# Performance work log

Hardware: AMD Instinct MI355X
Metric: run time of the kernel (lower is better)

## Reference

```python
import jax, jax.numpy as jnp
import numpy as np

N_QUBITS = 10
N_LAYERS = 3
DIM = 2 ** N_QUBITS
B = 2048
T1, T2, GATE_TIME = 0.05, 0.07, 1e-07
P_GATE_1Q, P_GATE_2Q, P_READOUT = 0.001, 0.01, 0.02
P_AMP = 1.0 - np.exp(-GATE_TIME / T1)
P_PHASE = 1.0 - np.exp(-GATE_TIME / T2)

_I = np.eye(2, dtype=np.complex64)
_X = np.array([[0, 1], [1, 0]], np.complex64)
_Y = np.array([[0, -1j], [1j, 0]], np.complex64)
_Z = np.array([[1, 0], [0, -1]], np.complex64)

def _depol(p):
    return [np.sqrt(1 - p) * _I, np.sqrt(p / 3) * _X, np.sqrt(p / 3) * _Y, np.sqrt(p / 3) * _Z]

def _ampdamp(g):
    return [np.array([[1, 0], [0, np.sqrt(1 - g)]], np.complex64), np.array([[0, np.sqrt(g)], [0, 0]], np.complex64)]

def _phasedamp(g):
    return [np.array([[1, 0], [0, np.sqrt(1 - g)]], np.complex64), np.array([[0, 0], [0, np.sqrt(g)]], np.complex64)]

def _bitflip(p):
    return [np.sqrt(1 - p) * _I, np.sqrt(p) * _X]

DEPOL1 = [jnp.asarray(k) for k in _depol(P_GATE_1Q)]
DEPOL2 = [jnp.asarray(k) for k in _depol(P_GATE_2Q)]
AMP = [jnp.asarray(k) for k in _ampdamp(P_AMP)]
PHASE = [jnp.asarray(k) for k in _phasedamp(P_PHASE)]
BITFLIP = [jnp.asarray(k) for k in _bitflip(P_READOUT)]
CNOT = jnp.asarray(np.array([[1, 0, 0, 0], [0, 1, 0, 0], [0, 0, 0, 1], [0, 0, 1, 0]], np.complex64).reshape(2, 2, 2, 2))

def pauli_strings(n):
    out = []
    for q in range(n):
        for ch in 'XZ':
            out.append('I' * q + ch + 'I' * (n - q - 1))
    return out

def pauli_tensor(strings):
    mats = {'I': np.eye(2), 'X': np.array([[0., 1.], [1., 0.]]), 'Z': np.array([[1., 0.], [0., -1.]])}
    Ps = []
    for s in strings:
        P = np.array([[1.0]])
        for ch in s:
            P = np.kron(P, mats[ch])
        Ps.append(P)
    return np.stack(Ps).astype(np.float32)

def _apply1(rho, K, q, n):
    # rho' = K rho K^dagger on wire q; rho has shape (2,)*2n (ket axes 0..n-1, bra axes n..2n-1)
    rho = jnp.moveaxis(jnp.tensordot(K, rho, axes=[[1], [q]]), 0, q)
    rho = jnp.moveaxis(jnp.tensordot(jnp.conj(K), rho, axes=[[1], [n + q]]), 0, n + q)
    return rho

def _apply2(rho, U, q1, q2, n):
    rho = jnp.moveaxis(jnp.tensordot(U, rho, axes=[[2, 3], [q1, q2]]), [0, 1], [q1, q2])
    rho = jnp.moveaxis(jnp.tensordot(jnp.conj(U), rho, axes=[[2, 3], [n + q1, n + q2]]), [0, 1], [n + q1, n + q2])
    return rho

def _chan1(rho, Ks, q, n):
    out = _apply1(rho, Ks[0], q, n)
    for K in Ks[1:]:
        out = out + _apply1(rho, K, q, n)
    return out

def _rot(phi, theta, omega):
    # qml.Rot = RZ(omega) @ RY(theta) @ RZ(phi)
    c = jnp.cos(theta / 2).astype(jnp.complex64)
    s = jnp.sin(theta / 2).astype(jnp.complex64)
    ep = jnp.exp(-0.5j * (phi + omega))
    em = jnp.exp(0.5j * (phi - omega))
    return jnp.stack([jnp.stack([ep * c, -em * s]), jnp.stack([jnp.conj(em) * s, jnp.conj(ep) * c])])

def _simulate(weights):
    nl, nq, _ = weights.shape
    rho = jnp.zeros((2,) * (2 * nq), jnp.complex64).at[(0,) * (2 * nq)].set(1.0)
    for l in range(nl):
        for q in range(nq):
            rho = _apply1(rho, _rot(weights[l, q, 0], weights[l, q, 1], weights[l, q, 2]), q, nq)
            rho = _chan1(rho, DEPOL1, q, nq)
            rho = _chan1(rho, AMP, q, nq)
            rho = _chan1(rho, PHASE, q, nq)
        for q in range(nq):
            t = (q + 1) % nq
            rho = _apply2(rho, CNOT, q, t, nq)
            for wq in (q, t):
                rho = _chan1(rho, DEPOL2, wq, nq)
            for wq in (q, t):
                rho = _chan1(rho, AMP, wq, nq)
            for wq in (q, t):
                rho = _chan1(rho, PHASE, wq, nq)
    for q in range(nq):
        rho = _chan1(rho, BITFLIP, q, nq)
    return rho.reshape(2 ** nq, 2 ** nq)

def setup_inputs() -> dict:
    key = jax.random.key(0)
    k1, k2, k3 = jax.random.split(key, 3)
    x = jax.random.normal(k1, (B, DIM), jnp.float32)
    circuit_weights = jax.random.uniform(k2, (N_LAYERS, N_QUBITS, 3), jnp.float32)
    w = jax.random.normal(k3, (2 * N_QUBITS,), jnp.float32) * 0.01
    b = jnp.zeros((DIM,), jnp.float32)
    P_tensor = jnp.asarray(pauli_tensor(pauli_strings(N_QUBITS)))  # [K, dim, dim]
    return {"x": x, "b": b, "w": w, "circuit_weights": circuit_weights, "P_tensor": P_tensor}

def reference(x, b, w, circuit_weights, P_tensor):
    x_t = x + b  # [B, dim]
    feats = jnp.einsum('bm,kmn,bn->bk', x_t, P_tensor, x_t)  # [B, K]
    rho = _simulate(circuit_weights)  # [dim, dim] complex
    exps = jnp.real(jnp.einsum('kmn,nm->k', P_tensor.astype(jnp.complex64), rho))  # tr(P_k rho)
    logits = jnp.sum(feats * (w * exps), axis=1)
    return jax.nn.sigmoid(logits)
```

## Files before the change

kernel.cpp:

```cpp
#include <hip/hip_runtime.h>
#include <hip/hip_bf16.h>
#include <math.h>

struct cf { float x, y; };
__device__ __forceinline__ cf cfmul(cf a, cf b){ return {a.x*b.x - a.y*b.y, a.x*b.y + a.y*b.x}; }
__device__ __forceinline__ cf cfconj(cf a){ return {a.x, -a.y}; }
__device__ __forceinline__ cf cfadd(cf a, cf b){ return {a.x+b.x, a.y+b.y}; }

__device__ __forceinline__ void pmat(int k, cf* P){
    if (k==0){ P[0]={1.f,0.f}; P[1]={0.f,0.f}; P[2]={0.f,0.f}; P[3]={1.f,0.f}; }
    else if (k==1){ P[0]={0.f,0.f}; P[1]={1.f,0.f}; P[2]={1.f,0.f}; P[3]={0.f,0.f}; }
    else if (k==2){ P[0]={0.f,0.f}; P[1]={0.f,-1.f}; P[2]={0.f,1.f}; P[3]={0.f,0.f}; }
    else { P[0]={1.f,0.f}; P[1]={0.f,0.f}; P[2]={0.f,0.f}; P[3]={-1.f,0.f}; }
}
__device__ void mul2(cf* C, const cf* A, const cf* B){
    C[0]=cfadd(cfmul(A[0],B[0]),cfmul(A[1],B[2]));
    C[1]=cfadd(cfmul(A[0],B[1]),cfmul(A[1],B[3]));
    C[2]=cfadd(cfmul(A[2],B[0]),cfmul(A[3],B[2]));
    C[3]=cfadd(cfmul(A[2],B[1]),cfmul(A[3],B[3]));
}
__device__ void ptm_acc(float* T, const cf* K){
    cf Kd[4] = {cfconj(K[0]), cfconj(K[2]), cfconj(K[1]), cfconj(K[3])};
    for (int s=0;s<4;s++){
        cf Ps[4]; pmat(s,Ps);
        cf t1[4], t2[4];
        mul2(t1, K, Ps);
        mul2(t2, t1, Kd);
        for (int t=0;t<4;t++){
            cf Pt[4]; pmat(t,Pt);
            float re = Pt[0].x*t2[0].x - Pt[0].y*t2[0].y
                     + Pt[1].x*t2[2].x - Pt[1].y*t2[2].y
                     + Pt[2].x*t2[1].x - Pt[2].y*t2[1].y
                     + Pt[3].x*t2[3].x - Pt[3].y*t2[3].y;
            T[t*4+s] += 0.5f*re;
        }
    }
}
__device__ void rmm4(float* C, const float* A, const float* B){
    for (int i=0;i<4;i++) for (int j=0;j<4;j++){
        float s=0.f;
        for (int k=0;k<4;k++) s += A[i*4+k]*B[k*4+j];
        C[i*4+j]=s;
    }
}

__device__ void prep_compute(float* sm, const float* __restrict__ wts, int tid){
    if (tid < 31){
        const float GA = -expm1f(-2.0000000000000002e-06f);
        const float GP = -expm1f(-1.4285714285714286e-06f);
        float sa = sqrtf(1.f-GA), spp = sqrtf(1.f-GP);
        float p = (tid==30) ? 0.01f : 0.001f;
        float f = 1.f - (4.f/3.f)*p;
        float Tn[16] = {0};
        Tn[0]      = 1.f;
        Tn[1*4+1]  = spp*sa*f;
        Tn[2*4+2]  = spp*sa*f;
        Tn[3*4+3]  = (1.f-GA)*f;
        Tn[3*4+0]  = GA;
        if (tid == 30){
            for (int i=0;i<16;i++) sm[480+i] = Tn[i];
        } else {
            float phi = wts[tid*3+0], th = wts[tid*3+1], om = wts[tid*3+2];
            float ct = cosf(0.5f*th), st = sinf(0.5f*th);
            cf ep = {cosf(0.5f*(phi+om)), -sinf(0.5f*(phi+om))};
            cf em = {cosf(0.5f*(phi-om)),  sinf(0.5f*(phi-om))};
            cf U[4];
            U[0] = { ep.x*ct,  ep.y*ct};
            U[1] = {-em.x*st, -em.y*st};
            U[2] = { em.x*st, -em.y*st};
            U[3] = { ep.x*ct, -ep.y*ct};
            float Tr[16] = {0};
            ptm_acc(Tr, U);
            float S[16]; rmm4(S, Tn, Tr);
            for (int i=0;i<16;i++) sm[tid*16+i] = S[i];
        }
    }
}

__device__ __forceinline__ unsigned swz(unsigned t){ return t ^ ((t>>7)&0x1Cu); }

#define ALONG_A(Mp) { _Pragma("unroll") for (int db_=0; db_<4; db_++){ \
    float a0=v[db_], a1=v[4+db_], a2=v[8+db_], a3=v[12+db_]; \
    _Pragma("unroll") for (int dp_=0; dp_<4; dp_++){ \
        v[dp_*4+db_] = (Mp)[dp_*4+0]*a0 + (Mp)[dp_*4+1]*a1 + (Mp)[dp_*4+2]*a2 + (Mp)[dp_*4+3]*a3; } } }

#define ALONG_B(Mp) { _Pragma("unroll") for (int da_=0; da_<4; da_++){ \
    float a0=v[da_*4+0], a1=v[da_*4+1], a2=v[da_*4+2], a3=v[da_*4+3]; \
    _Pragma("unroll") for (int dp_=0; dp_<4; dp_++){ \
        v[da_*4+dp_] = (Mp)[dp_*4+0]*a0 + (Mp)[dp_*4+1]*a1 + (Mp)[dp_*4+2]*a2 + (Mp)[dp_*4+3]*a3; } } }

#define ALONG_AT(Mp) { _Pragma("unroll") for (int db_=0; db_<4; db_++){ \
    float a0=v[db_], a1=v[4+db_], a2=v[8+db_], a3=v[12+db_]; \
    _Pragma("unroll") for (int dp_=0; dp_<4; dp_++){ \
        v[dp_*4+db_] = (Mp)[0*4+dp_]*a0 + (Mp)[1*4+dp_]*a1 + (Mp)[2*4+dp_]*a2 + (Mp)[3*4+dp_]*a3; } } }

#define ALONG_BT(Mp) { _Pragma("unroll") for (int da_=0; da_<4; da_++){ \
    float a0=v[da_*4+0], a1=v[da_*4+1], a2=v[da_*4+2], a3=v[da_*4+3]; \
    _Pragma("unroll") for (int dp_=0; dp_<4; dp_++){ \
        v[da_*4+dp_] = (Mp)[0*4+dp_]*a0 + (Mp)[1*4+dp_]*a1 + (Mp)[2*4+dp_]*a2 + (Mp)[3*4+dp_]*a3; } } }

#define CNOT_PERM { float t0; \
    t0=v[4];  v[4]=v[5];   v[5]=t0;  \
    t0=v[8];  v[8]=v[9];   v[9]=t0;  \
    t0=v[2];  v[2]=v[14];  v[14]=t0; \
    t0=v[3];  v[3]=v[15];  v[15]=t0; \
    t0=v[6];  v[6]=v[11];  v[11]=t0; \
    t0=v[7];  v[7]=-v[10]; v[10]=-t0; }

__device__ __constant__ const int cA_PA[5] = {0,10,8,6,4}, cA_PB[5] = {10,8,6,4,2};
__device__ __constant__ const int cB_PA[5] = {2,10,8,6,4}, cB_PB[5] = {10,8,6,4,0};

template<int LAYER, int ISB>
__device__ __forceinline__ void run_ops(float* tile, const float* sm, int tid){
#pragma unroll
    for (int i=0; i<5; i++){
        const int pa = ISB ? cB_PA[i] : cA_PA[i];
        const int pb = ISB ? cB_PB[i] : cA_PB[i];
        const int mA = (!ISB && i==0) ? LAYER*160 : -1;
        const int mB = !ISB ? (LAYER*10 + i + 1)*16
                            : ((i < 4) ? (LAYER*10 + 6 + i)*16 : -1);
        const int lo = pa < pb ? pa : pb, hi = pa < pb ? pb : pa;
        unsigned g8 = (unsigned)tid;
        unsigned xx = ((g8 >> lo) << (lo+2)) | (g8 & ((1u<<lo)-1u));
        xx = ((xx >> hi) << (hi+2)) | (xx & ((1u<<hi)-1u));
        unsigned adr[16];
        float v[16];
#pragma unroll
        for (int d=0; d<16; d++){
            unsigned t = xx | ((unsigned)(d>>2) << pa) | ((unsigned)(d&3) << pb);
            adr[d] = swz(t);
            v[d] = tile[adr[d]];
        }
        if (mA >= 0){ const float* M = sm + mA; ALONG_A(M); }
        if (mB >= 0){ const float* M = sm + mB; ALONG_B(M); }
        CNOT_PERM
        { const float* M = sm + 480; ALONG_B(M); ALONG_A(M); }
#pragma unroll
        for (int d=0; d<16; d++) tile[adr[d]] = v[d];
        __syncthreads();
    }
}

__global__ void __launch_bounds__(512, 1)
phase0_dual(float* __restrict__ rho, const float* __restrict__ wts,
            float* __restrict__ smg, float* __restrict__ Vbuf)
{
    __shared__ __align__(16) float tileS[4096];
    __shared__ __align__(16) float tileV[4096];
    __shared__ __align__(16) float sm[496];
    int tid = threadIdx.x;
    unsigned blk = blockIdx.x;
    const bool lower = (tid < 256);
    const int lt = tid & 255;

    prep_compute(sm, wts, tid);

    if (lower){
        unsigned bo = blk << 12;
#pragma unroll
        for (int r=0; r<16; r++){
            unsigned u = lt + 256u*r;
            unsigned g = u | bo;
            unsigned e = g & 0x55555u, o = (g>>1) & 0x55555u;
            tileS[swz(u)] = (e==o) ? 1.f : 0.f;
        }
    } else if (blk < 12){
        int k = (int)blk;
        unsigned sk = ((k & 1) ? 3u : 1u) << (2*(k>>1));
#pragma unroll
        for (int r=0; r<16; r++){
            unsigned u = lt + 256u*r;
            tileV[swz(u)] = (u == sk) ? 1.f : 0.f;
        }
    }
    __syncthreads();

    if (blk == 0 && lower && lt < 124)
        reinterpret_cast<float4*>(smg)[lt] = *reinterpret_cast<const float4*>(&sm[4*lt]);

#pragma unroll
    for (int it=0; it<5; ++it){
        if (lower){
            const int i = it;
            const int pa = cA_PA[i], pb = cA_PB[i];
            const int mA = (i==0) ? 0 : -1;
            const int mB = (i + 1)*16;
            const int lo = pa < pb ? pa : pb, hi = pa < pb ? pb : pa;
            unsigned g8 = (unsigned)lt;
            unsigned xx = ((g8 >> lo) << (lo+2)) | (g8 & ((1u<<lo)-1u));
            xx = ((xx >> hi) << (hi+2)) | (xx & ((1u<<hi)-1u));
            unsigned adr[16];
            float v[16];
#pragma unroll
            for (int d=0; d<16; d++){
                unsigned t = xx | ((unsigned)(d>>2) << pa) | ((unsigned)(d&3) << pb);
                adr[d] = swz(t);
                v[d] = tileS[adr[d]];
            }
            if (mA >= 0){ const float* M = sm + mA; ALONG_A(M); }
            { const float* M = sm + mB; ALONG_B(M); }
            CNOT_PERM
            { const float* M = sm + 480; ALONG_B(M); ALONG_A(M); }
#pragma unroll
            for (int d=0; d<16; d++) tileS[adr[d]] = v[d];
        } else if (blk < 12){
            const int i = 4 - it;
            const int pa = cB_PA[i], pb = cB_PB[i];
            const int mB = (i < 4) ? (26 + i)*16 : -1;
            const int lo = pa < pb ? pa : pb, hi = pa < pb ? pb : pa;
            unsigned g8 = (unsigned)lt;
            unsigned xx = ((g8 >> lo) << (lo+2)) | (g8 & ((1u<<lo)-1u));
            xx = ((xx >> hi) << (hi+2)) | (xx & ((1u<<hi)-1u));
            unsigned adr[16];
            float v[16];
#pragma unroll
            for (int d=0; d<16; d++){
                unsigned t = xx | ((unsigned)(d>>2) << pa) | ((unsigned)(d&3) << pb);
                adr[d] = swz(t);
                v[d] = tileV[adr[d]];
            }
            { const float* M = sm + 480; ALONG_AT(M); ALONG_BT(M); }
            CNOT_PERM
            if (mB >= 0){ const float* M = sm + mB; ALONG_BT(M); }
#pragma unroll
            for (int d=0; d<16; d++) tileV[adr[d]] = v[d];
        }
        __syncthreads();
    }

    if (lower){
        unsigned bo = blk << 12;
#pragma unroll
        for (int r=0; r<4; r++){
            unsigned u = 4u*(lt + 256u*r);
            *reinterpret_cast<float4*>(rho + (u | bo)) =
                *reinterpret_cast<const float4*>(&tileS[swz(u)]);
        }
    } else if (blk < 12){
#pragma unroll
        for (int r=0; r<4; r++){
            unsigned u = 4u*(lt + 256u*r);
            *reinterpret_cast<float4*>(Vbuf + (int)blk*4096 + u) =
                *reinterpret_cast<const float4*>(&tileV[swz(u)]);
        }
    }
}

template<int LAYER, int ISB, int MODE>
__global__ void __launch_bounds__(256)
fused6(float* __restrict__ rho, const float* __restrict__ smg, float* __restrict__ cvec,
       const float* __restrict__ Vbuf, float* __restrict__ part)
{
    __shared__ __align__(16) float tile[4096];
    __shared__ __align__(16) float sm[496];
    __shared__ float redp[192];
    int tid = threadIdx.x;
    unsigned blk = blockIdx.x;

    if (tid < 124)
        reinterpret_cast<float4*>(sm)[tid] = reinterpret_cast<const float4*>(smg)[tid];

    unsigned bo = blk << (ISB ? 4 : 12);
#pragma unroll
    for (int r=0; r<4; r++){
        unsigned u = 4u*(tid + 256u*r);
        unsigned g = ISB ? ((u & 15u) | ((u>>4)<<12) | bo) : (u | bo);
        *reinterpret_cast<float4*>(&tile[swz(u)]) = *reinterpret_cast<const float4*>(rho + g);
    }
    __syncthreads();

    run_ops<LAYER, ISB>(tile, sm, tid);

    if (MODE == 3){
        if (blk == 0 && tid < 8){
            const unsigned TI[8] = {1024u,3072u,256u,768u,64u,192u,16u,48u};
            cvec[2 + tid] = tile[swz(TI[tid])];
        }
        if (tid < 192){
            int k = tid >> 4, j = tid & 15;
            redp[tid] = Vbuf[k*4096 + (int)blk*16 + j] * tile[j];
        }
        __syncthreads();
        if (tid < 12){
            float s = 0.f;
#pragma unroll
            for (int j=0; j<16; j++) s += redp[tid*16 + j];
            part[tid*256 + (int)blk] = s;
        }
        return;
    }

#pragma unroll
    for (int r=0; r<4; r++){
        unsigned u = 4u*(tid + 256u*r);
        unsigned g = ISB ? ((u & 15u) | ((u>>4)<<12) | bo) : (u | bo);
        *reinterpret_cast<float4*>(rho + g) = *reinterpret_cast<const float4*>(&tile[swz(u)]);
    }
}

__global__ void __launch_bounds__(256)
logits_mega(const float* __restrict__ part, const float* __restrict__ cvec,
            const float* __restrict__ x, const float* __restrict__ bvec,
            const float* __restrict__ w, float* __restrict__ out)
{
    __shared__ float xs[1024];
    __shared__ float cvw[20];
    __shared__ float redl[80];
    __shared__ float redp[192];
    int tid = threadIdx.x;
    int b = (int)blockIdx.x;

    if (tid < 192){
        int k = tid >> 4, j = tid & 15;
        float s = 0.f;
#pragma unroll
        for (int m=0; m<16; m++) s += part[k*256 + j*16 + m];
        redp[tid] = s;
    }
    {
        float4 xv = reinterpret_cast<const float4*>(x + (size_t)b*1024)[tid];
        float4 bv = reinterpret_cast<const float4*>(bvec)[tid];
        xs[tid*4+0] = xv.x + bv.x;
        xs[tid*4+1] = xv.y + bv.y;
        xs[tid*4+2] = xv.z + bv.z;
        xs[tid*4+3] = xv.w + bv.w;
    }
    __syncthreads();
    if (tid < 12){
        float s = 0.f;
#pragma unroll
        for (int j=0; j<16; j++) s += redp[tid*16 + j];
        const int TQ[6] = {0,5,9,8,7,6};
        int ci = 2*TQ[tid>>1] + (tid & 1);
        cvw[ci] = ((tid & 1) ? 0.96f : 1.0f) * w[ci] * s;
    } else if (tid < 20){
        int ci = tid - 10;
        cvw[ci] = ((ci & 1) ? 0.96f : 1.0f) * w[ci] * cvec[ci];
    }

    float aX[10] = {0,0,0,0,0,0,0,0,0,0};
    float aZ[10] = {0,0,0,0,0,0,0,0,0,0};
#pragma unroll
    for (int r=0; r<4; r++){
        int m = tid + r*256;
        float xm = xs[m];
        float x2 = xm*xm;
#pragma unroll
        for (int q=0; q<10; q++){
            int bit = 1 << (9-q);
            aX[q] += xm * xs[m ^ bit];
            aZ[q] += (m & bit) ? -x2 : x2;
        }
    }
    int lane = tid & 63, wv = tid >> 6;
#pragma unroll
    for (int kk=0; kk<20; kk++){
        float v = (kk < 10) ? aX[kk] : aZ[kk-10];
        v += __shfl_down(v, 32); v += __shfl_down(v, 16); v += __shfl_down(v, 8);
        v += __shfl_down(v, 4);  v += __shfl_down(v, 2);  v += __shfl_down(v, 1);
        if (lane == 0) redl[wv*20 + kk] = v;
    }
    __syncthreads();
    if (tid == 0){
        float logit = 0.f;
#pragma unroll
        for (int q=0; q<10; q++){
            float FX = redl[q]    + redl[20+q] + redl[40+q] + redl[60+q];
            float FZ = redl[10+q] + redl[30+q] + redl[50+q] + redl[70+q];
            logit += cvw[2*q] * FX + cvw[2*q+1] * FZ;
        }
        out[b] = 1.f / (1.f + expf(-logit));
    }
}

extern "C" void kernel_launch(void* const* d_in, const int* in_sizes, int n_in,
                              void* d_out, int out_size, void* d_ws, size_t ws_size,
                              hipStream_t stream) {
    const float* x    = (const float*)d_in[0];
    const float* bvec = (const float*)d_in[1];
    const float* w    = (const float*)d_in[2];
    const float* cw   = (const float*)d_in[3];
    float* out = (float*)d_out;

    char* ws = (char*)d_ws;
    float* rho  = (float*)ws;
    float* smg  = (float*)(ws + (size_t)(1u<<20)*sizeof(float));
    float* cvec = smg + 512;
    float* part = cvec + 32;
    float* Vbuf = part + 3072;
    (void)ws_size; (void)in_sizes; (void)n_in; (void)out_size;

    phase0_dual<<<256, 512, 0, stream>>>(rho, cw, smg, Vbuf);
    fused6<0,1,0><<<256, 256, 0, stream>>>(rho, smg, cvec, Vbuf, part);
    fused6<1,0,0><<<256, 256, 0, stream>>>(rho, smg, cvec, Vbuf, part);
    fused6<1,1,0><<<256, 256, 0, stream>>>(rho, smg, cvec, Vbuf, part);
    fused6<2,0,3><<<256, 256, 0, stream>>>(rho, smg, cvec, Vbuf, part);
    logits_mega<<<2048, 256, 0, stream>>>(part, cvec, x, bvec, w, out);
}
```

Measured before the change: 67.96 us.

## Fold last circuit layer into precomputed adjoint observables to drop one pass

Removes the final fused6 launch, which applied the last layer to the full density matrix. Instead, phase0 precomputes extra back-propagated basis tensors (P4Tbuf, VAbuf), and the third-layer kernel contracts its tile against them to produce all twenty expectation partials directly. This saves one full read-modify-write pass over rho and one launch. In exchange it adds a heavier per-block contraction (a 16x16 inner product per output plus 12 Vbuf reads per element) and more precompute blocks in phase0.

```diff
diff --git a/kernel.cpp b/kernel.cpp
--- a/kernel.cpp
+++ b/kernel.cpp
@@ -143,7 +143,8 @@
 
 __global__ void __launch_bounds__(512, 1)
 phase0_dual(float* __restrict__ rho, const float* __restrict__ wts,
-            float* __restrict__ smg, float* __restrict__ Vbuf)
+            float* __restrict__ smg, float* __restrict__ Vbuf,
+            float* __restrict__ P4Tbuf, float* __restrict__ VAbuf)
 {
     __shared__ __align__(16) float tileS[4096];
     __shared__ __align__(16) float tileV[4096];
@@ -164,9 +165,16 @@
             unsigned e = g & 0x55555u, o = (g>>1) & 0x55555u;
             tileS[swz(u)] = (e==o) ? 1.f : 0.f;
         }
-    } else if (blk < 12){
-        int k = (int)blk;
-        unsigned sk = ((k & 1) ? 3u : 1u) << (2*(k>>1));
+    } else if (blk < 36){
+        unsigned sk;
+        if (blk < 12){
+            sk = (((blk & 1u) ? 3u : 1u) << (2*(blk>>1)));
+        } else if (blk < 28){
+            sk = blk - 12u;
+        } else {
+            unsigned j = blk - 28u;
+            sk = (((j & 1u) ? 3u : 1u) << (2*(6 - ((j>>1)+1))));
+        }
 #pragma unroll
         for (int r=0; r<16; r++){
             unsigned u = lt + 256u*r;
@@ -203,10 +211,11 @@
             { const float* M = sm + 480; ALONG_B(M); ALONG_A(M); }
 #pragma unroll
             for (int d=0; d<16; d++) tileS[adr[d]] = v[d];
-        } else if (blk < 12){
+        } else if (blk < 36){
+            const bool bch = (blk < 12);
             const int i = 4 - it;
-            const int pa = cB_PA[i], pb = cB_PB[i];
-            const int mB = (i < 4) ? (26 + i)*16 : -1;
+            const int pa = bch ? cB_PA[i] : cA_PA[i];
+            const int pb = bch ? cB_PB[i] : cA_PB[i];
             const int lo = pa < pb ? pa : pb, hi = pa < pb ? pb : pa;
             unsigned g8 = (unsigned)lt;
             unsigned xx = ((g8 >> lo) << (lo+2)) | (g8 & ((1u<<lo)-1u));
@@ -221,7 +230,9 @@
             }
             { const float* M = sm + 480; ALONG_AT(M); ALONG_BT(M); }
             CNOT_PERM
+            const int mB = bch ? ((i < 4) ? (26 + i)*16 : -1) : (21 + i)*16;
             if (mB >= 0){ const float* M = sm + mB; ALONG_BT(M); }
+            if (!bch && i == 0){ const float* M = sm + 320; ALONG_AT(M); }
 #pragma unroll
             for (int d=0; d<16; d++) tileV[adr[d]] = v[d];
         }
@@ -236,11 +247,14 @@
             *reinterpret_cast<float4*>(rho + (u | bo)) =
                 *reinterpret_cast<const float4*>(&tileS[swz(u)]);
         }
-    } else if (blk < 12){
+    } else if (blk < 36){
+        float* dst = (blk < 12) ? (Vbuf + (int)blk*4096)
+                   : (blk < 28) ? (P4Tbuf + ((int)blk-12)*4096)
+                                : (VAbuf + ((int)blk-28)*4096);
 #pragma unroll
         for (int r=0; r<4; r++){
             unsigned u = 4u*(lt + 256u*r);
-            *reinterpret_cast<float4*>(Vbuf + (int)blk*4096 + u) =
+            *reinterpret_cast<float4*>(dst + u) =
                 *reinterpret_cast<const float4*>(&tileV[swz(u)]);
         }
     }
@@ -248,12 +262,12 @@
 
 template<int LAYER, int ISB, int MODE>
 __global__ void __launch_bounds__(256)
-fused6(float* __restrict__ rho, const float* __restrict__ smg, float* __restrict__ cvec,
-       const float* __restrict__ Vbuf, float* __restrict__ part)
+fused6(float* __restrict__ rho, const float* __restrict__ smg,
+       const float* __restrict__ Vbuf, const float* __restrict__ P4Tbuf,
+       const float* __restrict__ VAbuf, float* __restrict__ part)
 {
     __shared__ __align__(16) float tile[4096];
     __shared__ __align__(16) float sm[496];
-    __shared__ float redp[192];
     int tid = threadIdx.x;
     unsigned blk = blockIdx.x;
 
@@ -271,22 +285,44 @@
 
     run_ops<LAYER, ISB>(tile, sm, tid);
 
-    if (MODE == 3){
-        if (blk == 0 && tid < 8){
-            const unsigned TI[8] = {1024u,3072u,256u,768u,64u,192u,16u,48u};
-            cvec[2 + tid] = tile[swz(TI[tid])];
-        }
-        if (tid < 192){
-            int k = tid >> 4, j = tid & 15;
-            redp[tid] = Vbuf[k*4096 + (int)blk*16 + j] * tile[j];
-        }
+    if (MODE == 4){
+        __shared__ float p4tb[256];
+        __shared__ float redva[128];
+        __shared__ float redw[48];
+        p4tb[tid] = P4Tbuf[(tid>>4)*4096 + (int)blk*16 + (tid&15)];
+        if (tid < 128)
+            redva[tid] = VAbuf[(tid>>4)*4096 + (int)blk*16 + (tid&15)] * tile[swz((unsigned)(tid&15))];
         __syncthreads();
-        if (tid < 12){
+        if (tid < 8){
             float s = 0.f;
 #pragma unroll
-            for (int j=0; j<16; j++) s += redp[tid*16 + j];
-            part[tid*256 + (int)blk] = s;
-        }
+            for (int e=0;e<16;e++) s += redva[tid*16+e];
+            part[(12+tid)*256 + (int)blk] = s;
+        }
+        float sk[12];
+#pragma unroll
+        for (int k=0;k<12;k++) sk[k] = 0.f;
+        const float* pr = &p4tb[(tid&15)*16];
+        for (int j=0;j<16;j++){
+            int d9876 = (tid>>4) + 16*j;
+            float A = 0.f;
+#pragma unroll
+            for (int e=0;e<16;e++) A += pr[e] * tile[swz((unsigned)(e | (d9876<<4)))];
+            int vidx = tid + (j<<8);
+#pragma unroll
+            for (int k=0;k<12;k++) sk[k] += Vbuf[k*4096 + vidx] * A;
+        }
+        int lane = tid & 63, wv = tid >> 6;
+#pragma unroll
+        for (int k=0;k<12;k++){
+            float v = sk[k];
+            v += __shfl_down(v,32); v += __shfl_down(v,16); v += __shfl_down(v,8);
+            v += __shfl_down(v,4);  v += __shfl_down(v,2);  v += __shfl_down(v,1);
+            if (lane == 0) redw[wv*12 + k] = v;
+        }
+        __syncthreads();
+        if (tid < 12)
+            part[tid*256 + (int)blk] = redw[tid] + redw[12+tid] + redw[24+tid] + redw[36+tid];
         return;
     }
 
@@ -299,22 +335,22 @@
 }
 
 __global__ void __launch_bounds__(256)
-logits_mega(const float* __restrict__ part, const float* __restrict__ cvec,
+logits_mega(const float* __restrict__ part,
             const float* __restrict__ x, const float* __restrict__ bvec,
             const float* __restrict__ w, float* __restrict__ out)
 {
     __shared__ float xs[1024];
     __shared__ float cvw[20];
     __shared__ float redl[80];
-    __shared__ float redp[192];
+    __shared__ float redp[160];
     int tid = threadIdx.x;
     int b = (int)blockIdx.x;
 
-    if (tid < 192){
-        int k = tid >> 4, j = tid & 15;
+    if (tid < 160){
+        int k = tid >> 3, m = tid & 7;
         float s = 0.f;
 #pragma unroll
-        for (int m=0; m<16; m++) s += part[k*256 + j*16 + m];
+        for (int i=0; i<32; i++) s += part[k*256 + m*32 + i];
         redp[tid] = s;
     }
     {
@@ -326,16 +362,15 @@
         xs[tid*4+3] = xv.w + bv.w;
     }
     __syncthreads();
-    if (tid < 12){
+    if (tid < 20){
         float s = 0.f;
 #pragma unroll
-        for (int j=0; j<16; j++) s += redp[tid*16 + j];
+        for (int m=0; m<8; m++) s += redp[tid*8 + m];
         const int TQ[6] = {0,5,9,8,7,6};
-        int ci = 2*TQ[tid>>1] + (tid & 1);
-        cvw[ci] = ((tid & 1) ? 0.96f : 1.0f) * w[ci] * s;
-    } else if (tid < 20){
-        int ci = tid - 10;
-        cvw[ci] = ((ci & 1) ? 0.96f : 1.0f) * w[ci] * cvec[ci];
+        int ci;
+        if (tid < 12) ci = 2*TQ[tid>>1] + (tid & 1);
+        else { int j = tid - 12; ci = 2*((j>>1)+1) + (j & 1); }
+        cvw[ci] = ((ci & 1) ? 0.96f : 1.0f) * w[ci] * s;
     }
 
     float aX[10] = {0,0,0,0,0,0,0,0,0,0};
@@ -383,17 +418,17 @@
     float* out = (float*)d_out;
 
     char* ws = (char*)d_ws;
-    float* rho  = (float*)ws;
-    float* smg  = (float*)(ws + (size_t)(1u<<20)*sizeof(float));
-    float* cvec = smg + 512;
-    float* part = cvec + 32;
-    float* Vbuf = part + 3072;
+    float* rho    = (float*)ws;
+    float* smg    = (float*)(ws + (size_t)(1u<<20)*sizeof(float));
+    float* part   = smg + 512;
+    float* Vbuf   = part + 5120;
+    float* P4Tbuf = Vbuf + 12*4096;
+    float* VAbuf  = P4Tbuf + 16*4096;
     (void)ws_size; (void)in_sizes; (void)n_in; (void)out_size;
 
-    phase0_dual<<<256, 512, 0, stream>>>(rho, cw, smg, Vbuf);
-    fused6<0,1,0><<<256, 256, 0, stream>>>(rho, smg, cvec, Vbuf, part);
-    fused6<1,0,0><<<256, 256, 0, stream>>>(rho, smg, cvec, Vbuf, part);
-    fused6<1,1,0><<<256, 256, 0, stream>>>(rho, smg, cvec, Vbuf, part);
-    fused6<2,0,3><<<256, 256, 0, stream>>>(rho, smg, cvec, Vbuf, part);
-    logits_mega<<<2048, 256, 0, stream>>>(part, cvec, x, bvec, w, out);
-}
+    phase0_dual<<<256, 512, 0, stream>>>(rho, cw, smg, Vbuf, P4Tbuf, VAbuf);
+    fused6<0,1,0><<<256, 256, 0, stream>>>(rho, smg, Vbuf, P4Tbuf, VAbuf, part);
+    fused6<1,0,0><<<256, 256, 0, stream>>>(rho, smg, Vbuf, P4Tbuf, VAbuf, part);
+    fused6<1,1,4><<<256, 256, 0, stream>>>(rho, smg, Vbuf, P4Tbuf, VAbuf, part);
+    logits_mega<<<2048, 256, 0, stream>>>(part, x, bvec, w, out);
+}
```

Measured after the change: 70.78 us. 4.2% more time.
